# Kernel tuning notes

Measured on AMD Instinct MI355X. Metric: run time of the kernel, lower is better.

Reference implementation:

```python
import math
import jax, jax.numpy as jnp
import numpy as np

B, L, E, H = 8, 1024, 512, 8
HD = E // H  # head_dim = 64
P = 2 * L - 1  # relative position length


def setup_inputs() -> dict:
    key = jax.random.key(0)
    ks = jax.random.split(key, 9)
    s = 0.02  # xavier-ish scale for params
    return {
        "x": jax.random.normal(ks[0], (B, L, E), jnp.float32),
        "pos_embs": jax.random.normal(ks[1], (1, P, E), jnp.float32),
        "in_proj_weight": jax.random.normal(ks[2], (3 * E, E), jnp.float32) * s,
        "linear_pos_w": jax.random.normal(ks[3], (E, E), jnp.float32) * s,
        "out_proj_w": jax.random.normal(ks[4], (E, E), jnp.float32) * s,
        "out_proj_b": jnp.zeros((E,), jnp.float32),
        "pos_bias_u": jax.random.normal(ks[5], (HD, H), jnp.float32) * s,
        "pos_bias_v": jax.random.normal(ks[6], (HD, H), jnp.float32) * s,
    }


def rel_shift(t):
    # Transformer-XL relative shift: pad/reshape/slice trick.
    b, h, q, p = t.shape  # p = 2*klen - 1
    t = jnp.pad(t, ((0, 0), (0, 0), (0, 0), (1, 0)))
    t = t.reshape(b, h, p + 1, q)[:, :, 1:, :].reshape(b, h, q, p)
    return t[..., : p // 2 + 1]  # (b, h, q, klen)


def reference(x, pos_embs, in_proj_weight, linear_pos_w, out_proj_w, out_proj_b,
              pos_bias_u, pos_bias_v):
    bsz, qlen, _ = x.shape
    scale = 1.0 / math.sqrt(E)  # note: 1/sqrt(embed_dim), not head_dim

    # fused qkv projection; torch chunks along the last dim of (B,L,H,3*HD)
    proj = (x @ in_proj_weight.T).reshape(bsz, qlen, H, 3 * HD)
    q, k, v = jnp.split(proj, 3, axis=-1)  # each (B,L,H,HD)

    # positional keys
    p_k = (pos_embs @ linear_pos_w.T).reshape(-1, H, HD)  # (P,H,HD)

    # pos_bias_u is stored (HD,H) and .view(H,HD)'d in torch -> plain reshape
    u = pos_bias_u.reshape(H, HD)
    vb = pos_bias_v.reshape(H, HD)

    matrix_ac = jnp.einsum('bqhd,bkhd->bhqk', (q + u) * scale, k)
    matrix_bd = jnp.einsum('bqhd,phd->bhqp', (q + vb) * scale, p_k)
    matrix_bd = rel_shift(matrix_bd)  # (B,H,L,L)

    attn = jax.nn.softmax((matrix_ac + matrix_bd).astype(jnp.float32), axis=-1)

    ctx = jnp.einsum('bhqk,bkhd->bqhd', attn, v).reshape(bsz, qlen, E)
    out = ctx @ out_proj_w.T + out_proj_b
    return out, attn
```

## Files before the change

### kernel.cpp

```cpp
#include <hip/hip_runtime.h>
#include <math.h>

#define BB 8
#define LL 1024
#define EE 512
#define HH 8
#define HD 64
#define PP 2047

static constexpr float SCALE = 0.04419417382415922f;

typedef __bf16 bf16x8 __attribute__((ext_vector_type(8)));
typedef float f32x4 __attribute__((ext_vector_type(4)));
typedef unsigned short u16;
typedef u16 u16x8 __attribute__((ext_vector_type(8)));
typedef u16 u16x4 __attribute__((ext_vector_type(4)));

#define MFMA16(a, b, c) __builtin_amdgcn_mfma_f32_16x16x32_bf16(a, b, c, 0, 0, 0)

static __device__ __forceinline__ unsigned short f2bfbits(float f) {
    union { float f; unsigned u; } v; v.f = f;
    unsigned r = v.u + 0x7fffu + ((v.u >> 16) & 1u);
    return (unsigned short)(r >> 16);
}
static __device__ __forceinline__ float bfbits2f(unsigned short b) {
    union { unsigned u; float f; } v; v.u = ((unsigned)b) << 16;
    return v.f;
}

static __device__ __forceinline__ u16x8 cvt8(float4 lo, float4 hi) {
    u16x8 r;
    r[0] = f2bfbits(lo.x); r[1] = f2bfbits(lo.y);
    r[2] = f2bfbits(lo.z); r[3] = f2bfbits(lo.w);
    r[4] = f2bfbits(hi.x); r[5] = f2bfbits(hi.y);
    r[6] = f2bfbits(hi.z); r[7] = f2bfbits(hi.w);
    return r;
}

static __device__ __forceinline__ void gload_lds16(const u16* g, u16* l) {
    __builtin_amdgcn_global_load_lds(
        (const __attribute__((address_space(1))) unsigned int*)g,
        (__attribute__((address_space(3))) unsigned int*)l, 16, 0, 0);
}

__global__ __launch_bounds__(256) void cast_all(
    const float* __restrict__ x, const float* __restrict__ pe,
    const float* __restrict__ ipw, const float* __restrict__ lpw,
    const float* __restrict__ opw,
    u16* __restrict__ Xb, u16* __restrict__ Pb, u16* __restrict__ Wqb,
    u16* __restrict__ Wpb, u16* __restrict__ Wob)
{
    size_t e = ((size_t)blockIdx.x * 256 + threadIdx.x) * 8;
    const float* src; u16* dst; size_t off;
    if (e < 4194304)      { src = x;   dst = Xb;  off = e; }
    else if (e < 5242368) { src = pe;  dst = Pb;  off = e - 4194304; }
    else if (e < 6028800) { src = ipw; dst = Wqb; off = e - 5242368; }
    else if (e < 6290944) { src = lpw; dst = Wpb; off = e - 6028800; }
    else if (e < 6553088) { src = opw; dst = Wob; off = e - 6290944; }
    else return;
    float4 lo = *(const float4*)&src[off];
    float4 hi = *(const float4*)&src[off + 4];
    *(u16x8*)&dst[off] = cvt8(lo, hi);
}

template<bool CLAMP>
static __device__ __forceinline__ void gemm128b(
    const u16* __restrict__ Ab, const u16* __restrict__ Bb,
    int m0, int n0, int amax, u16* As, u16* Bs, f32x4 (&acc)[4][4])
{
    const int tid = threadIdx.x;
    const int w = tid >> 6, lane = tid & 63;
    const int g = lane >> 4, c16 = lane & 15;
    const int wr = w >> 1, wc = w & 1;

#pragma unroll
    for (int i = 0; i < 4; i++)
#pragma unroll
        for (int j = 0; j < 4; j++) acc[i][j] = (f32x4){0.f, 0.f, 0.f, 0.f};

    int arow[4], brow[4], cs8[4], ldsu[4];
#pragma unroll
    for (int j = 0; j < 4; j++) {
        int U = j * 256 + tid;
        int row = U >> 3, cu = U & 7;
        cs8[j] = (cu ^ (row & 7)) * 8;
        int ar = m0 + row;
        if (CLAMP) ar = ar > amax ? amax : ar;
        arow[j] = ar;
        brow[j] = n0 + row;
        ldsu[j] = (j * 256 + (w << 6)) * 8;
    }

    for (int kt = 0; kt < EE; kt += 64) {
#pragma unroll
        for (int j = 0; j < 4; j++) {
            gload_lds16(Ab + (size_t)arow[j] * EE + kt + cs8[j], As + ldsu[j]);
            gload_lds16(Bb + (size_t)brow[j] * EE + kt + cs8[j], Bs + ldsu[j]);
        }
        __syncthreads();
#pragma unroll
        for (int kk = 0; kk < 2; kk++) {
            bf16x8 av[4], bv[4];
#pragma unroll
            for (int mt = 0; mt < 4; mt++) {
                int r0 = wr * 64 + mt * 16 + c16;
                av[mt] = *(const bf16x8*)&As[r0 * 64 + (((kk * 4 + g) ^ (r0 & 7)) << 3)];
            }
#pragma unroll
            for (int nt = 0; nt < 4; nt++) {
                int r0 = wc * 64 + nt * 16 + c16;
                bv[nt] = *(const bf16x8*)&Bs[r0 * 64 + (((kk * 4 + g) ^ (r0 & 7)) << 3)];
            }
#pragma unroll
            for (int mt = 0; mt < 4; mt++)
#pragma unroll
                for (int nt = 0; nt < 4; nt++)
                    acc[mt][nt] = MFMA16(av[mt], bv[nt], acc[mt][nt]);
        }
        __syncthreads();
    }
}

__global__ __launch_bounds__(256) void qkvpos_kernel(
    const u16* __restrict__ xb,
    const u16* __restrict__ wq,
    const float* __restrict__ ubias,
    const float* __restrict__ vbias,
    unsigned short* __restrict__ Qu,
    unsigned short* __restrict__ Qv,
    unsigned short* __restrict__ Kw,
    unsigned short* __restrict__ Vt,
    const u16* __restrict__ peb,
    const u16* __restrict__ wp,
    unsigned short* __restrict__ pko)
{
    __shared__ u16 As[128 * 64];
    __shared__ u16 Bs[128 * 64];
    const int bid = blockIdx.x;
    const int tid = threadIdx.x;
    const int w = tid >> 6, lane = tid & 63;
    const int g = lane >> 4, c16 = lane & 15;
    const int wr = w >> 1, wc = w & 1;
    f32x4 acc[4][4];

    if (bid < 768) {
        const int xcd = bid & 7, j = bid >> 3;
        const int m0 = (xcd * 8 + j / 12) * 128, n0 = (j % 12) * 128;
        gemm128b<false>(xb, wq, m0, n0, 0, As, Bs, acc);
#pragma unroll
        for (int mt = 0; mt < 4; mt++) {
#pragma unroll
            for (int r = 0; r < 4; r++) {
                int m = m0 + wr * 64 + mt * 16 + g * 4 + r;
                int b = m >> 10, l = m & 1023;
#pragma unroll
                for (int nt = 0; nt < 4; nt++) {
                    int n = n0 + wc * 64 + nt * 16 + c16;
                    int h = n / 192;
                    int rr = n - h * 192;
                    int cls = rr >> 6;
                    int d = rr & 63;
                    float v = acc[mt][nt][r];
                    if (cls == 0) {
                        size_t idx = ((size_t)(b * HH + h) * LL + l) * HD + d;
                        Qu[idx] = f2bfbits((v + ubias[h * 64 + d]) * SCALE);
                        Qv[idx] = f2bfbits((v + vbias[h * 64 + d]) * SCALE);
                    } else if (cls == 1) {
                        Kw[((size_t)(b * HH + h) * LL + l) * HD + d] = f2bfbits(v);
                    } else {
                        Vt[((size_t)(b * HH + h) * HD + d) * LL + l] = f2bfbits(v);
                    }
                }
            }
        }
    } else {
        const int j = bid - 768;
        const int m0 = (j >> 2) * 128, n0 = (j & 3) * 128;
        gemm128b<true>(peb, wp, m0, n0, PP - 1, As, Bs, acc);
#pragma unroll
        for (int mt = 0; mt < 4; mt++) {
#pragma unroll
            for (int r = 0; r < 4; r++) {
                int p = m0 + wr * 64 + mt * 16 + g * 4 + r;
                if (p >= PP) continue;
#pragma unroll
                for (int nt = 0; nt < 4; nt++) {
                    int n = n0 + wc * 64 + nt * 16 + c16;
                    int h = n >> 6, d = n & 63;
                    pko[((size_t)h * PP + p) * HD + d] = f2bfbits(acc[mt][nt][r]);
                }
            }
        }
    }
}

__global__ __launch_bounds__(256) void outproj_kernel(
    const u16* __restrict__ ctxb,
    const u16* __restrict__ wo,
    const float* __restrict__ bias,
    float* __restrict__ out)
{
    __shared__ u16 As[128 * 64];
    __shared__ u16 Bs[128 * 64];
    const int bid = blockIdx.x;
    const int xcd = bid & 7, j = bid >> 3;
    const int m0 = (xcd * 8 + (j >> 2)) * 128, n0 = (j & 3) * 128;
    f32x4 acc[4][4];
    gemm128b<false>(ctxb, wo, m0, n0, 0, As, Bs, acc);

    const int tid = threadIdx.x;
    const int w = tid >> 6, lane = tid & 63;
    const int g = lane >> 4, c16 = lane & 15;
    const int wr = w >> 1, wc = w & 1;

#pragma unroll
    for (int mt = 0; mt < 4; mt++) {
#pragma unroll
        for (int r = 0; r < 4; r++) {
            int m = m0 + wr * 64 + mt * 16 + g * 4 + r;
#pragma unroll
            for (int nt = 0; nt < 4; nt++) {
                int n = n0 + wc * 64 + nt * 16 + c16;
                __builtin_nontemporal_store(acc[mt][nt][r] + bias[n],
                                            &out[(size_t)m * EE + n]);
            }
        }
    }
}

__global__ __launch_bounds__(256, 4) void attn_kernel(
    const unsigned short* __restrict__ Qu, const unsigned short* __restrict__ Qv,
    const unsigned short* __restrict__ Kw, const unsigned short* __restrict__ Vt,
    const unsigned short* __restrict__ pk,
    float* __restrict__ attn,
    u16* __restrict__ ctxb)
{
    const int bid = blockIdx.x;
    const int xcd = bid & 7, jj = bid >> 3;
    const int bh = xcd * 8 + (jj >> 6);
    const int q0 = (jj & 63) * 16;
    const int b = bh >> 3, h = bh & 7;
    const int tid = threadIdx.x;
    const int w = tid >> 6, lane = tid & 63;
    const int g = lane >> 4, c16 = lane & 15;

    __shared__ __align__(16) unsigned char SH[4][4864];
    __shared__ float SMmax[4][16];
    __shared__ float SMsum[4][16];
    unsigned short* BDGw = (unsigned short*)SH[w];

    const unsigned short* qub = Qu + ((size_t)bh * LL + q0 + c16) * HD + g * 8;
    const unsigned short* qvb = Qv + ((size_t)bh * LL + q0 + c16) * HD + g * 8;
    bf16x8 au0 = *(const bf16x8*)qub;
    bf16x8 au1 = *(const bf16x8*)(qub + 32);
    bf16x8 av0 = *(const bf16x8*)qvb;
    bf16x8 av1 = *(const bf16x8*)(qvb + 32);

    f32x4 lg[16];
#pragma unroll
    for (int t = 0; t < 16; t++) lg[t] = (f32x4){0.f, 0.f, 0.f, 0.f};

    const unsigned short* kbase  = Kw + (size_t)bh * LL * HD;
    const unsigned short* pkbase = pk + (size_t)h * PP * HD;

#pragma unroll
    for (int p = 0; p < 2; p++) {
        const int kp = w * 256 + p * 128;
        const int pstart = kp - q0 + 1008;
#pragma unroll
        for (int ct = 0; ct < 9; ct++) {
            int prow = pstart + ct * 16 + c16;
            prow = prow > (PP - 1) ? (PP - 1) : prow;
            const unsigned short* pb = pkbase + (size_t)prow * HD + g * 8;
            f32x4 acc = (f32x4){0.f, 0.f, 0.f, 0.f};
            acc = MFMA16(av0, *(const bf16x8*)pb, acc);
            acc = MFMA16(av1, *(const bf16x8*)(pb + 32), acc);
#pragma unroll
            for (int r = 0; r < 4; r++)
                BDGw[(g * 4 + r) * 152 + ct * 16 + c16] = f2bfbits(acc[r]);
        }
#pragma unroll
        for (int jt = 0; jt < 8; jt++) {
            const unsigned short* kb = kbase + (size_t)(kp + jt * 16 + c16) * HD + g * 8;
            int t = p * 8 + jt;
            lg[t] = MFMA16(au0, *(const bf16x8*)kb, lg[t]);
            lg[t] = MFMA16(au1, *(const bf16x8*)(kb + 32), lg[t]);
        }
        __syncthreads();
#pragma unroll
        for (int jt = 0; jt < 8; jt++) {
            int t = p * 8 + jt;
#pragma unroll
            for (int r = 0; r < 4; r++) {
                int i = g * 4 + r;
                int c = jt * 16 + c16 - i + 15;
                lg[t][r] += bfbits2f(BDGw[i * 152 + c]);
            }
        }
        __syncthreads();
    }

    float M[4], Sv[4], inv[4];
#pragma unroll
    for (int r = 0; r < 4; r++) {
        float m = lg[0][r];
#pragma unroll
        for (int t = 1; t < 16; t++) m = fmaxf(m, lg[t][r]);
        M[r] = m;
    }
#pragma unroll
    for (int off = 8; off >= 1; off >>= 1)
#pragma unroll
        for (int r = 0; r < 4; r++) M[r] = fmaxf(M[r], __shfl_xor(M[r], off, 16));
    if (c16 == 0) {
#pragma unroll
        for (int r = 0; r < 4; r++) SMmax[w][g * 4 + r] = M[r];
    }
    __syncthreads();
#pragma unroll
    for (int r = 0; r < 4; r++) {
        int row = g * 4 + r;
        M[r] = fmaxf(fmaxf(SMmax[0][row], SMmax[1][row]),
                     fmaxf(SMmax[2][row], SMmax[3][row]));
        Sv[r] = 0.f;
    }
#pragma unroll
    for (int t = 0; t < 16; t++)
#pragma unroll
        for (int r = 0; r < 4; r++) {
            float e = __expf(lg[t][r] - M[r]);
            lg[t][r] = e;
            Sv[r] += e;
        }
#pragma unroll
    for (int off = 8; off >= 1; off >>= 1)
#pragma unroll
        for (int r = 0; r < 4; r++) Sv[r] += __shfl_xor(Sv[r], off, 16);
    if (c16 == 0) {
#pragma unroll
        for (int r = 0; r < 4; r++) SMsum[w][g * 4 + r] = Sv[r];
    }
    __syncthreads();
#pragma unroll
    for (int r = 0; r < 4; r++) {
        int row = g * 4 + r;
        inv[r] = 1.0f / (SMsum[0][row] + SMsum[1][row] + SMsum[2][row] + SMsum[3][row]);
    }

    float* arow = attn + (size_t)bh * LL * LL;
#pragma unroll
    for (int t = 0; t < 16; t++)
#pragma unroll
        for (int r = 0; r < 4; r++) {
            float pr = lg[t][r] * inv[r];
            lg[t][r] = pr;
            __builtin_nontemporal_store(
                pr, &arow[(size_t)(q0 + g * 4 + r) * LL + w * 256 + t * 16 + c16]);
        }

    f32x4 cacc[4];
#pragma unroll
    for (int nt = 0; nt < 4; nt++) cacc[nt] = (f32x4){0.f, 0.f, 0.f, 0.f};

#pragma unroll
    for (int p = 0; p < 2; p++) {
        const int kp = w * 256 + p * 128;
        __syncthreads();
#pragma unroll
        for (int jt = 0; jt < 8; jt++) {
            int t = p * 8 + jt;
#pragma unroll
            for (int r = 0; r < 4; r++)
                BDGw[(g * 4 + r) * 152 + jt * 16 + c16] = f2bfbits(lg[t][r]);
        }
        __syncthreads();
        bf16x8 pa[4];
#pragma unroll
        for (int kk = 0; kk < 4; kk++)
            pa[kk] = *(const bf16x8*)&BDGw[c16 * 152 + kk * 32 + g * 8];
#pragma unroll
        for (int kk = 0; kk < 4; kk++) {
#pragma unroll
            for (int nt = 0; nt < 4; nt++) {
                const unsigned short* vb =
                    Vt + ((size_t)bh * HD + nt * 16 + c16) * LL + kp + kk * 32 + g * 8;
                cacc[nt] = MFMA16(pa[kk], *(const bf16x8*)vb, cacc[nt]);
            }
        }
    }

    __syncthreads();
    {
        float* CTXw = (float*)SH[w];
#pragma unroll
        for (int nt = 0; nt < 4; nt++)
#pragma unroll
            for (int r = 0; r < 4; r++)
                CTXw[(g * 4 + r) * 68 + nt * 16 + c16] = cacc[nt][r];
    }
    __syncthreads();
    {
        int row = tid >> 4, d4 = (tid & 15) * 4;
        f32x4 s = *(const f32x4*)&((const float*)SH[0])[row * 68 + d4];
        s += *(const f32x4*)&((const float*)SH[1])[row * 68 + d4];
        s += *(const f32x4*)&((const float*)SH[2])[row * 68 + d4];
        s += *(const f32x4*)&((const float*)SH[3])[row * 68 + d4];
        u16x4 o;
        o[0] = f2bfbits(s[0]); o[1] = f2bfbits(s[1]);
        o[2] = f2bfbits(s[2]); o[3] = f2bfbits(s[3]);
        *(u16x4*)&ctxb[((size_t)b * LL + q0 + row) * EE + h * HD + d4] = o;
    }
}

extern "C" void kernel_launch(void* const* d_in, const int* in_sizes, int n_in,
                              void* d_out, int out_size, void* d_ws, size_t ws_size,
                              hipStream_t stream)
{
    const float* x   = (const float*)d_in[0];
    const float* pe  = (const float*)d_in[1];
    const float* ipw = (const float*)d_in[2];
    const float* lpw = (const float*)d_in[3];
    const float* opw = (const float*)d_in[4];
    const float* opb = (const float*)d_in[5];
    const float* pbu = (const float*)d_in[6];
    const float* pbv = (const float*)d_in[7];

    float* out  = (float*)d_out;
    float* attn = (float*)d_out + (size_t)BB * LL * EE;

    const size_t NQ = (size_t)BB * HH * LL * HD;
    u16* wsu  = (u16*)d_ws;
    u16* ctxb = wsu; wsu += (size_t)BB * LL * EE;
    u16* Qu   = wsu; wsu += NQ;
    u16* Qv   = wsu; wsu += NQ;
    u16* Kw   = wsu; wsu += NQ;
    u16* Vt   = wsu; wsu += NQ;
    u16* pkb  = wsu; wsu += (size_t)HH * PP * HD;
    u16* Xb   = wsu; wsu += 4194304;
    u16* Pb   = wsu; wsu += 1048064;
    u16* Wqb  = wsu; wsu += 786432;
    u16* Wpb  = wsu; wsu += 262144;
    u16* Wob  = wsu; wsu += 262144;

    cast_all<<<3200, 256, 0, stream>>>(x, pe, ipw, lpw, opw, Xb, Pb, Wqb, Wpb, Wob);
    qkvpos_kernel<<<832, 256, 0, stream>>>(Xb, Wqb, pbu, pbv, Qu, Qv, Kw, Vt,
                                           Pb, Wpb, pkb);
    attn_kernel<<<4096, 256, 0, stream>>>(Qu, Qv, Kw, Vt, pkb, attn, ctxb);
    outproj_kernel<<<256, 256, 0, stream>>>(ctxb, Wob, opb, out);
}
```

Measured before the change: 523.3 us.

## Recompute attention logits in a two-pass softmax and stage the V transpose through LDS

The attention kernel no longer keeps all 64 logits per thread in registers. It computes per-half online max/sum statistics in a first pass, then recomputes the QK and positional MFMAs in a second pass to produce probabilities, streaming them to the output and into a small LDS buffer for the PV MFMA. Block-wide syncs become wave-local fences, and launch bounds are raised to 5 blocks per CU to improve occupancy, at the cost of doing the score MFMAs twice. The QKV projection now transposes V through swizzled shared memory so it can issue vectorized coalesced stores, and the attn and out stores drop the nontemporal hint.

```diff
diff --git a/kernel.cpp b/kernel.cpp
--- a/kernel.cpp
+++ b/kernel.cpp
@@ -41,6 +41,11 @@
     __builtin_amdgcn_global_load_lds(
         (const __attribute__((address_space(1))) unsigned int*)g,
         (__attribute__((address_space(3))) unsigned int*)l, 16, 0, 0);
+}
+
+static __device__ __forceinline__ void wave_fence() {
+    asm volatile("s_waitcnt lgkmcnt(0)" ::: "memory");
+    __builtin_amdgcn_sched_barrier(0);
 }
 
 __global__ __launch_bounds__(256) void cast_all(
@@ -134,8 +139,9 @@
     const u16* __restrict__ wp,
     unsigned short* __restrict__ pko)
 {
-    __shared__ u16 As[128 * 64];
-    __shared__ u16 Bs[128 * 64];
+    __shared__ u16 S[2 * 128 * 64];
+    u16* As = S;
+    u16* Bs = S + 128 * 64;
     const int bid = blockIdx.x;
     const int tid = threadIdx.x;
     const int w = tid >> 6, lane = tid & 63;
@@ -168,9 +174,24 @@
                     } else if (cls == 1) {
                         Kw[((size_t)(b * HH + h) * LL + l) * HD + d] = f2bfbits(v);
                     } else {
-                        Vt[((size_t)(b * HH + h) * HD + d) * LL + l] = f2bfbits(v);
+                        int nl = n - n0;
+                        int ml = m - m0;
+                        S[nl * 128 + (ml ^ ((nl & 7) << 3))] = f2bfbits(v);
                     }
                 }
+            }
+        }
+        __syncthreads();
+        const int b0 = m0 >> 10, l0 = m0 & 1023;
+#pragma unroll
+        for (int pp = 0; pp < 8; pp++) {
+            int nl = pp * 16 + (tid >> 4);
+            int n = n0 + nl;
+            int h = n / 192, rr = n - h * 192;
+            if (rr >= 128) {
+                int d = rr & 63, mu = tid & 15;
+                u16x8 vv = *(const u16x8*)&S[nl * 128 + ((mu * 8) ^ ((nl & 7) << 3))];
+                *(u16x8*)&Vt[((size_t)(b0 * HH + h) * HD + d) * LL + l0 + mu * 8] = vv;
             }
         }
     } else {
@@ -200,13 +221,12 @@
     const float* __restrict__ bias,
     float* __restrict__ out)
 {
-    __shared__ u16 As[128 * 64];
-    __shared__ u16 Bs[128 * 64];
+    __shared__ u16 S[2 * 128 * 64];
     const int bid = blockIdx.x;
     const int xcd = bid & 7, j = bid >> 3;
     const int m0 = (xcd * 8 + (j >> 2)) * 128, n0 = (j & 3) * 128;
     f32x4 acc[4][4];
-    gemm128b<false>(ctxb, wo, m0, n0, 0, As, Bs, acc);
+    gemm128b<false>(ctxb, wo, m0, n0, 0, S, S + 128 * 64, acc);
 
     const int tid = threadIdx.x;
     const int w = tid >> 6, lane = tid & 63;
@@ -221,17 +241,16 @@
 #pragma unroll
             for (int nt = 0; nt < 4; nt++) {
                 int n = n0 + wc * 64 + nt * 16 + c16;
-                __builtin_nontemporal_store(acc[mt][nt][r] + bias[n],
-                                            &out[(size_t)m * EE + n]);
-            }
-        }
-    }
-}
-
-__global__ __launch_bounds__(256, 4) void attn_kernel(
-    const unsigned short* __restrict__ Qu, const unsigned short* __restrict__ Qv,
-    const unsigned short* __restrict__ Kw, const unsigned short* __restrict__ Vt,
-    const unsigned short* __restrict__ pk,
+                out[(size_t)m * EE + n] = acc[mt][nt][r] + bias[n];
+            }
+        }
+    }
+}
+
+__global__ __launch_bounds__(256, 5) void attn_kernel(
+    const u16* __restrict__ Qu, const u16* __restrict__ Qv,
+    const u16* __restrict__ Kw, const u16* __restrict__ Vt,
+    const u16* __restrict__ pk,
     float* __restrict__ attn,
     u16* __restrict__ ctxb)
 {
@@ -244,25 +263,24 @@
     const int w = tid >> 6, lane = tid & 63;
     const int g = lane >> 4, c16 = lane & 15;
 
-    __shared__ __align__(16) unsigned char SH[4][4864];
+    __shared__ __align__(16) u16 BDG[4][16 * 152];
+    __shared__ __align__(16) u16 PBUF[4][16 * 40];
     __shared__ float SMmax[4][16];
     __shared__ float SMsum[4][16];
-    unsigned short* BDGw = (unsigned short*)SH[w];
-
-    const unsigned short* qub = Qu + ((size_t)bh * LL + q0 + c16) * HD + g * 8;
-    const unsigned short* qvb = Qv + ((size_t)bh * LL + q0 + c16) * HD + g * 8;
+    u16* BDGw = BDG[w];
+    u16* PBw  = PBUF[w];
+
+    const u16* qub = Qu + ((size_t)bh * LL + q0 + c16) * HD + g * 8;
+    const u16* qvb = Qv + ((size_t)bh * LL + q0 + c16) * HD + g * 8;
     bf16x8 au0 = *(const bf16x8*)qub;
     bf16x8 au1 = *(const bf16x8*)(qub + 32);
     bf16x8 av0 = *(const bf16x8*)qvb;
     bf16x8 av1 = *(const bf16x8*)(qvb + 32);
 
-    f32x4 lg[16];
-#pragma unroll
-    for (int t = 0; t < 16; t++) lg[t] = (f32x4){0.f, 0.f, 0.f, 0.f};
-
-    const unsigned short* kbase  = Kw + (size_t)bh * LL * HD;
-    const unsigned short* pkbase = pk + (size_t)h * PP * HD;
-
+    const u16* kbase  = Kw + (size_t)bh * LL * HD;
+    const u16* pkbase = pk + (size_t)h * PP * HD;
+
+    float mh[2][4], sh[2][4];
 #pragma unroll
     for (int p = 0; p < 2; p++) {
         const int kp = w * 256 + p * 128;
@@ -271,7 +289,7 @@
         for (int ct = 0; ct < 9; ct++) {
             int prow = pstart + ct * 16 + c16;
             prow = prow > (PP - 1) ? (PP - 1) : prow;
-            const unsigned short* pb = pkbase + (size_t)prow * HD + g * 8;
+            const u16* pb = pkbase + (size_t)prow * HD + g * 8;
             f32x4 acc = (f32x4){0.f, 0.f, 0.f, 0.f};
             acc = MFMA16(av0, *(const bf16x8*)pb, acc);
             acc = MFMA16(av1, *(const bf16x8*)(pb + 32), acc);
@@ -279,119 +297,127 @@
             for (int r = 0; r < 4; r++)
                 BDGw[(g * 4 + r) * 152 + ct * 16 + c16] = f2bfbits(acc[r]);
         }
+        wave_fence();
+        f32x4 t8[8];
 #pragma unroll
         for (int jt = 0; jt < 8; jt++) {
-            const unsigned short* kb = kbase + (size_t)(kp + jt * 16 + c16) * HD + g * 8;
-            int t = p * 8 + jt;
-            lg[t] = MFMA16(au0, *(const bf16x8*)kb, lg[t]);
-            lg[t] = MFMA16(au1, *(const bf16x8*)(kb + 32), lg[t]);
-        }
-        __syncthreads();
-#pragma unroll
-        for (int jt = 0; jt < 8; jt++) {
-            int t = p * 8 + jt;
+            const u16* kb = kbase + (size_t)(kp + jt * 16 + c16) * HD + g * 8;
+            t8[jt] = (f32x4){0.f, 0.f, 0.f, 0.f};
+            t8[jt] = MFMA16(au0, *(const bf16x8*)kb, t8[jt]);
+            t8[jt] = MFMA16(au1, *(const bf16x8*)(kb + 32), t8[jt]);
+        }
+#pragma unroll
+        for (int jt = 0; jt < 8; jt++)
 #pragma unroll
             for (int r = 0; r < 4; r++) {
                 int i = g * 4 + r;
-                int c = jt * 16 + c16 - i + 15;
-                lg[t][r] += bfbits2f(BDGw[i * 152 + c]);
-            }
-        }
-        __syncthreads();
+                t8[jt][r] += bfbits2f(BDGw[i * 152 + jt * 16 + c16 - i + 15]);
+            }
+#pragma unroll
+        for (int r = 0; r < 4; r++) {
+            float m = t8[0][r];
+#pragma unroll
+            for (int jt = 1; jt < 8; jt++) m = fmaxf(m, t8[jt][r]);
+            float s = 0.f;
+#pragma unroll
+            for (int jt = 0; jt < 8; jt++) s += __expf(t8[jt][r] - m);
+            mh[p][r] = m;
+            sh[p][r] = s;
+        }
+        wave_fence();
     }
 
     float M[4], Sv[4], inv[4];
 #pragma unroll
     for (int r = 0; r < 4; r++) {
-        float m = lg[0][r];
-#pragma unroll
-        for (int t = 1; t < 16; t++) m = fmaxf(m, lg[t][r]);
-        M[r] = m;
+        float m2 = fmaxf(mh[0][r], mh[1][r]);
+        Sv[r] = sh[0][r] * __expf(mh[0][r] - m2) + sh[1][r] * __expf(mh[1][r] - m2);
+        M[r] = m2;
     }
 #pragma unroll
     for (int off = 8; off >= 1; off >>= 1)
 #pragma unroll
-        for (int r = 0; r < 4; r++) M[r] = fmaxf(M[r], __shfl_xor(M[r], off, 16));
+        for (int r = 0; r < 4; r++) {
+            float mo = __shfl_xor(M[r], off, 16);
+            float so = __shfl_xor(Sv[r], off, 16);
+            float mn = fmaxf(M[r], mo);
+            Sv[r] = Sv[r] * __expf(M[r] - mn) + so * __expf(mo - mn);
+            M[r] = mn;
+        }
     if (c16 == 0) {
 #pragma unroll
-        for (int r = 0; r < 4; r++) SMmax[w][g * 4 + r] = M[r];
+        for (int r = 0; r < 4; r++) {
+            SMmax[w][g * 4 + r] = M[r];
+            SMsum[w][g * 4 + r] = Sv[r];
+        }
     }
     __syncthreads();
 #pragma unroll
     for (int r = 0; r < 4; r++) {
         int row = g * 4 + r;
-        M[r] = fmaxf(fmaxf(SMmax[0][row], SMmax[1][row]),
-                     fmaxf(SMmax[2][row], SMmax[3][row]));
-        Sv[r] = 0.f;
-    }
-#pragma unroll
-    for (int t = 0; t < 16; t++)
-#pragma unroll
-        for (int r = 0; r < 4; r++) {
-            float e = __expf(lg[t][r] - M[r]);
-            lg[t][r] = e;
-            Sv[r] += e;
-        }
-#pragma unroll
-    for (int off = 8; off >= 1; off >>= 1)
-#pragma unroll
-        for (int r = 0; r < 4; r++) Sv[r] += __shfl_xor(Sv[r], off, 16);
-    if (c16 == 0) {
-#pragma unroll
-        for (int r = 0; r < 4; r++) SMsum[w][g * 4 + r] = Sv[r];
-    }
-    __syncthreads();
-#pragma unroll
-    for (int r = 0; r < 4; r++) {
-        int row = g * 4 + r;
-        inv[r] = 1.0f / (SMsum[0][row] + SMsum[1][row] + SMsum[2][row] + SMsum[3][row]);
-    }
-
+        float ma = SMmax[0][row], mb = SMmax[1][row];
+        float mc = SMmax[2][row], md = SMmax[3][row];
+        float mm = fmaxf(fmaxf(ma, mb), fmaxf(mc, md));
+        float ss = SMsum[0][row] * __expf(ma - mm) + SMsum[1][row] * __expf(mb - mm)
+                 + SMsum[2][row] * __expf(mc - mm) + SMsum[3][row] * __expf(md - mm);
+        M[r] = mm;
+        inv[r] = 1.0f / ss;
+    }
+
+    f32x4 cacc[4];
+#pragma unroll
+    for (int nt = 0; nt < 4; nt++) cacc[nt] = (f32x4){0.f, 0.f, 0.f, 0.f};
     float* arow = attn + (size_t)bh * LL * LL;
-#pragma unroll
-    for (int t = 0; t < 16; t++)
-#pragma unroll
-        for (int r = 0; r < 4; r++) {
-            float pr = lg[t][r] * inv[r];
-            lg[t][r] = pr;
-            __builtin_nontemporal_store(
-                pr, &arow[(size_t)(q0 + g * 4 + r) * LL + w * 256 + t * 16 + c16]);
-        }
-
-    f32x4 cacc[4];
-#pragma unroll
-    for (int nt = 0; nt < 4; nt++) cacc[nt] = (f32x4){0.f, 0.f, 0.f, 0.f};
 
 #pragma unroll
     for (int p = 0; p < 2; p++) {
         const int kp = w * 256 + p * 128;
-        __syncthreads();
-#pragma unroll
-        for (int jt = 0; jt < 8; jt++) {
-            int t = p * 8 + jt;
+        const int pstart = kp - q0 + 1008;
+#pragma unroll
+        for (int ct = 0; ct < 9; ct++) {
+            int prow = pstart + ct * 16 + c16;
+            prow = prow > (PP - 1) ? (PP - 1) : prow;
+            const u16* pb = pkbase + (size_t)prow * HD + g * 8;
+            f32x4 acc = (f32x4){0.f, 0.f, 0.f, 0.f};
+            acc = MFMA16(av0, *(const bf16x8*)pb, acc);
+            acc = MFMA16(av1, *(const bf16x8*)(pb + 32), acc);
 #pragma unroll
             for (int r = 0; r < 4; r++)
-                BDGw[(g * 4 + r) * 152 + jt * 16 + c16] = f2bfbits(lg[t][r]);
-        }
-        __syncthreads();
-        bf16x8 pa[4];
-#pragma unroll
-        for (int kk = 0; kk < 4; kk++)
-            pa[kk] = *(const bf16x8*)&BDGw[c16 * 152 + kk * 32 + g * 8];
-#pragma unroll
-        for (int kk = 0; kk < 4; kk++) {
+                BDGw[(g * 4 + r) * 152 + ct * 16 + c16] = f2bfbits(acc[r]);
+        }
+        wave_fence();
+#pragma unroll
+        for (int jt2 = 0; jt2 < 4; jt2++) {
+#pragma unroll
+            for (int e = 0; e < 2; e++) {
+                int jt = jt2 * 2 + e;
+                const u16* kb = kbase + (size_t)(kp + jt * 16 + c16) * HD + g * 8;
+                f32x4 t = (f32x4){0.f, 0.f, 0.f, 0.f};
+                t = MFMA16(au0, *(const bf16x8*)kb, t);
+                t = MFMA16(au1, *(const bf16x8*)(kb + 32), t);
+#pragma unroll
+                for (int r = 0; r < 4; r++) {
+                    int i = g * 4 + r;
+                    float s = t[r] + bfbits2f(BDGw[i * 152 + jt * 16 + c16 - i + 15]);
+                    float pr = __expf(s - M[r]) * inv[r];
+                    arow[(size_t)(q0 + i) * LL + kp + jt * 16 + c16] = pr;
+                    PBw[i * 40 + e * 16 + c16] = f2bfbits(pr);
+                }
+            }
+            wave_fence();
+            bf16x8 pa = *(const bf16x8*)&PBw[c16 * 40 + g * 8];
 #pragma unroll
             for (int nt = 0; nt < 4; nt++) {
-                const unsigned short* vb =
-                    Vt + ((size_t)bh * HD + nt * 16 + c16) * LL + kp + kk * 32 + g * 8;
-                cacc[nt] = MFMA16(pa[kk], *(const bf16x8*)vb, cacc[nt]);
-            }
-        }
-    }
-
-    __syncthreads();
+                const u16* vb = Vt + ((size_t)bh * HD + nt * 16 + c16) * LL
+                              + kp + jt2 * 32 + g * 8;
+                cacc[nt] = MFMA16(pa, *(const bf16x8*)vb, cacc[nt]);
+            }
+            wave_fence();
+        }
+    }
+
     {
-        float* CTXw = (float*)SH[w];
+        float* CTXw = (float*)BDGw;
 #pragma unroll
         for (int nt = 0; nt < 4; nt++)
 #pragma unroll
@@ -401,10 +427,10 @@
     __syncthreads();
     {
         int row = tid >> 4, d4 = (tid & 15) * 4;
-        f32x4 s = *(const f32x4*)&((const float*)SH[0])[row * 68 + d4];
-        s += *(const f32x4*)&((const float*)SH[1])[row * 68 + d4];
-        s += *(const f32x4*)&((const float*)SH[2])[row * 68 + d4];
-        s += *(const f32x4*)&((const float*)SH[3])[row * 68 + d4];
+        f32x4 s = *(const f32x4*)&((const float*)BDG[0])[row * 68 + d4];
+        s += *(const f32x4*)&((const float*)BDG[1])[row * 68 + d4];
+        s += *(const f32x4*)&((const float*)BDG[2])[row * 68 + d4];
+        s += *(const f32x4*)&((const float*)BDG[3])[row * 68 + d4];
         u16x4 o;
         o[0] = f2bfbits(s[0]); o[1] = f2bfbits(s[1]);
         o[2] = f2bfbits(s[2]); o[3] = f2bfbits(s[3]);
```

After: 802.1 us. +53.3%, slower.
